# Kernel optimization log

Measured on AMD Instinct MI355X. Metric: run time of the kernel, lower is better.

The kernel has to match this reference:

```python
import jax, jax.numpy as jnp
import numpy as np

BATCH, DIN, DSTATE, SEQLEN = 4, 2048, 16, 2048


def setup_inputs() -> dict:
    key = jax.random.key(0)
    ks = jax.random.split(key, 7)
    u = jax.random.normal(ks[0], (BATCH, DIN, SEQLEN), dtype=jnp.float32)
    # delta pre-softplus; moderate positive-ish values like Mamba dt_proj output
    delta = jax.random.uniform(ks[1], (BATCH, DIN, SEQLEN), dtype=jnp.float32, minval=-2.0, maxval=1.0)
    # A is negative in real Mamba (A = -exp(A_log)); keep recurrence stable
    A = -jnp.exp(jax.random.uniform(ks[2], (DIN, DSTATE), dtype=jnp.float32, minval=-1.0, maxval=1.0))
    B = jax.random.normal(ks[3], (BATCH, DSTATE, SEQLEN), dtype=jnp.float32)
    C = jax.random.normal(ks[4], (BATCH, DSTATE, SEQLEN), dtype=jnp.float32)
    D = jax.random.normal(ks[5], (DIN,), dtype=jnp.float32)
    z = jax.random.normal(ks[6], (BATCH, DIN, SEQLEN), dtype=jnp.float32)
    return {"u": u, "delta": delta, "A": A, "B": B, "C": C, "D": D, "z": z}


def reference(u, delta, A, B, C, D, z):
    """Mamba selective scan (selective_scan_ref semantics, delta_softplus=True).

    u, delta, z: (b, d, l); A: (d, n); B, C: (b, n, l); D: (d,).
    y_t = C_t . x_t + D*u_t, x_t = exp(dt_t*A)*x_{t-1} + dt_t*B_t*u_t,
    final y gated by SiLU(z).
    """
    dt = jax.nn.softplus(delta)                      # (b, d, l)

    def step(x, inp):
        dt_t, u_t, B_t, C_t = inp                    # (b,d) (b,d) (b,n) (b,n)
        dA = jnp.exp(dt_t[..., None] * A)            # (b, d, n)
        x = x * dA + (dt_t * u_t)[..., None] * B_t[:, None, :]
        y_t = jnp.einsum('bdn,bn->bd', x, C_t)
        return x, y_t

    xs = (jnp.moveaxis(dt, -1, 0),                   # (l, b, d)
          jnp.moveaxis(u, -1, 0),
          jnp.moveaxis(B, -1, 0),                    # (l, b, n)
          jnp.moveaxis(C, -1, 0))
    x0 = jnp.zeros((u.shape[0], u.shape[1], A.shape[1]), dtype=u.dtype)
    _, ys = jax.lax.scan(step, x0, xs)               # ys: (l, b, d)
    y = jnp.moveaxis(ys, 0, -1)                      # (b, d, l)
    y = y + D[None, :, None] * u
    y = y * (z * jax.nn.sigmoid(z))                  # SiLU gate
    return y
```

## Files before the change

kernel.cpp:

```cpp
#include <hip/hip_runtime.h>


#define BATCHSZ 4
#define DIN 2048
#define NSTATE 16
#define SEQ 2048
#define NCH (BATCHSZ * DIN)
#define NGRP (NCH / 256)
#define NC 16
#define LC (SEQ / NC)
#define SUB 32
#define NSUB (LC / SUB)
#define L2E 1.44269504f

__device__ __forceinline__ float softplus_f(float v) {
    float e = __builtin_amdgcn_exp2f(v * L2E);
    return 0.69314718f * __builtin_amdgcn_logf(1.0f + e);
}

__device__ __forceinline__ float silu_f(float v) {
    float s = __builtin_amdgcn_rcpf(1.0f + __builtin_amdgcn_exp2f(-v * L2E));
    return v * s;
}

__device__ __forceinline__ float comp4(const float4& f, int k) {
    return k == 0 ? f.x : k == 1 ? f.y : k == 2 ? f.z : f.w;
}

__device__ __forceinline__ void set4(float4& f, int k, float v) {
    if (k == 0) f.x = v; else if (k == 1) f.y = v; else if (k == 2) f.z = v; else f.w = v;
}

__device__ __forceinline__ void dma16(const float* g, float* l) {
    __builtin_amdgcn_global_load_lds(
        (const __attribute__((address_space(1))) void*)g,
        (__attribute__((address_space(3))) void*)l, 16, 0, 0);
}


__global__ __launch_bounds__(256) void k_transBC(
        const float* __restrict__ Bm, const float* __restrict__ Cm,
        float* __restrict__ Bt, float* __restrict__ Ct) {
    int idx = blockIdx.x * 256 + threadIdx.x;
    int b = idx >> 11;
    int t = idx & (SEQ - 1);
    const float* sb = Bm + (size_t)b * NSTATE * SEQ + t;
    const float* sc = Cm + (size_t)b * NSTATE * SEQ + t;
    float* db = Bt + ((size_t)b * SEQ + t) * NSTATE;
    float* dc = Ct + ((size_t)b * SEQ + t) * NSTATE;
    #pragma unroll
    for (int m = 0; m < 4; ++m) {
        float4 v, w;
        v.x = sb[(size_t)(m * 4 + 0) * SEQ]; w.x = sc[(size_t)(m * 4 + 0) * SEQ];
        v.y = sb[(size_t)(m * 4 + 1) * SEQ]; w.y = sc[(size_t)(m * 4 + 1) * SEQ];
        v.z = sb[(size_t)(m * 4 + 2) * SEQ]; w.z = sc[(size_t)(m * 4 + 2) * SEQ];
        v.w = sb[(size_t)(m * 4 + 3) * SEQ]; w.w = sc[(size_t)(m * 4 + 3) * SEQ];
        *(float4*)(db + m * 4) = v;
        *(float4*)(dc + m * 4) = w;
    }
}

__global__ __launch_bounds__(256, 4) void k_pass1(
        const float* __restrict__ u, const float* __restrict__ delta,
        const float* __restrict__ A, const float* __restrict__ Bt,
        float* __restrict__ wsq, float* __restrict__ wsS) {
    __shared__ float Ub[256 * 32];
    __shared__ float Db[256 * 32];

    int tid = threadIdx.x;
    int l = tid & 63;
    int w6 = tid & ~63;
    int g = blockIdx.x & (NGRP - 1);
    int c = blockIdx.x >> 5;
    int chBase = g << 8;
    int b = chBase >> 11;
    int bd = chBase + tid;
    int d = bd & (DIN - 1);
    int rowA = w6 + (l >> 3);
    int lq = l & 7;

    const float* ug = u + (size_t)chBase * SEQ + (size_t)c * LC;
    const float* dg = delta + (size_t)chBase * SEQ + (size_t)c * LC;
    const float* Btc = Bt + ((size_t)b * SEQ + (size_t)c * LC) * NSTATE;

    float A2[NSTATE];
    {
        const float* Ar = A + (size_t)d * NSTATE;
        #pragma unroll
        for (int n = 0; n < NSTATE; ++n) A2[n] = Ar[n] * L2E;
    }
    float x[NSTATE];
    #pragma unroll
    for (int n = 0; n < NSTATE; ++n) x[n] = 0.0f;
    float S = 0.0f;

    #pragma unroll
    for (int it = 0; it < 8; ++it) {
        int r = rowA + it * 8;
        int q = lq ^ (r & 7);
        dma16(ug + (size_t)r * SEQ + q * 4, &Ub[(w6 + it * 8) * 32]);
        dma16(dg + (size_t)r * SEQ + q * 4, &Db[(w6 + it * 8) * 32]);
    }

    for (int st = 0; st < NSUB; ++st) {
        asm volatile("s_waitcnt vmcnt(0)" ::: "memory");
        __builtin_amdgcn_sched_barrier(0);
        #pragma unroll
        for (int t4 = 0; t4 < 8; ++t4) {
            int ph = (t4 ^ (tid & 7)) * 4;
            float4 u4 = *(const float4*)(&Ub[tid * 32 + ph]);
            float4 d4 = *(const float4*)(&Db[tid * 32 + ph]);
            const float4* Br = (const float4*)(Btc + (size_t)(st * SUB + t4 * 4) * NSTATE);
            #pragma unroll
            for (int k = 0; k < 4; ++k) {
                float dt = softplus_f(comp4(d4, k));
                S += dt;
                float du = dt * comp4(u4, k);
                float bb[NSTATE];
                *(float4*)&bb[0] = Br[k * 4 + 0]; *(float4*)&bb[4] = Br[k * 4 + 1];
                *(float4*)&bb[8] = Br[k * 4 + 2]; *(float4*)&bb[12] = Br[k * 4 + 3];
                #pragma unroll
                for (int n = 0; n < NSTATE; ++n) {
                    float dA = __builtin_amdgcn_exp2f(A2[n] * dt);
                    x[n] = x[n] * dA + du * bb[n];
                }
            }
        }
        if (st + 1 < NSUB) {
            __builtin_amdgcn_sched_barrier(0);
            int tb = (st + 1) * SUB;
            #pragma unroll
            for (int it = 0; it < 8; ++it) {
                int r = rowA + it * 8;
                int q = lq ^ (r & 7);
                dma16(ug + (size_t)r * SEQ + tb + q * 4, &Ub[(w6 + it * 8) * 32]);
                dma16(dg + (size_t)r * SEQ + tb + q * 4, &Db[(w6 + it * 8) * 32]);
            }
        }
    }

    #pragma unroll
    for (int n = 0; n < NSTATE; ++n) wsq[((size_t)n * NC + c) * NCH + bd] = x[n];
    wsS[(size_t)c * NCH + bd] = S;
}

__global__ __launch_bounds__(256) void k_pass2(
        const float* __restrict__ A, float* __restrict__ wsq,
        float* __restrict__ wsS) {
    int idx = blockIdx.x * 256 + threadIdx.x;
    int n = idx >> 13;
    int bd = idx & (NCH - 1);
    int d = bd & (DIN - 1);

    float A2 = A[(size_t)d * NSTATE + n] * L2E;
    float x = 0.0f;
    float* qbase = wsq + (size_t)n * NC * NCH + bd;

    #pragma unroll
    for (int c0 = 0; c0 < NC; c0 += 4) {
        float S0 = wsS[(size_t)(c0 + 0) * NCH + bd];
        float S1 = wsS[(size_t)(c0 + 1) * NCH + bd];
        float S2 = wsS[(size_t)(c0 + 2) * NCH + bd];
        float S3 = wsS[(size_t)(c0 + 3) * NCH + bd];
        float* p0 = qbase + (size_t)(c0 + 0) * NCH;
        float* p1 = qbase + (size_t)(c0 + 1) * NCH;
        float* p2 = qbase + (size_t)(c0 + 2) * NCH;
        float* p3 = qbase + (size_t)(c0 + 3) * NCH;
        float q0 = *p0, q1 = *p1, q2 = *p2, q3 = *p3;
        float t0 = x; x = x * __builtin_amdgcn_exp2f(A2 * S0) + q0;
        float t1 = x; x = x * __builtin_amdgcn_exp2f(A2 * S1) + q1;
        float t2 = x; x = x * __builtin_amdgcn_exp2f(A2 * S2) + q2;
        float t3 = x; x = x * __builtin_amdgcn_exp2f(A2 * S3) + q3;
        *p0 = t0; *p1 = t1; *p2 = t2; *p3 = t3;
    }
}

__global__ __launch_bounds__(256, 4) void k_pass3(
        const float* __restrict__ u, const float* __restrict__ delta,
        const float* __restrict__ A, const float* __restrict__ Bt,
        const float* __restrict__ Ct, const float* __restrict__ Dv,
        const float* __restrict__ z, const float* __restrict__ wsq,
        float* __restrict__ out) {
    __shared__ float Ub[256 * 32];
    __shared__ float Db[256 * 32];

    int tid = threadIdx.x;
    int l = tid & 63;
    int w6 = tid & ~63;
    int g = blockIdx.x & (NGRP - 1);
    int c = blockIdx.x >> 5;
    int chBase = g << 8;
    int b = chBase >> 11;
    int bd = chBase + tid;
    int d = bd & (DIN - 1);
    int rowA = w6 + (l >> 3);
    int lq = l & 7;

    const float* ug = u + (size_t)chBase * SEQ + (size_t)c * LC;
    const float* dg = delta + (size_t)chBase * SEQ + (size_t)c * LC;
    const float* zg = z + (size_t)chBase * SEQ + (size_t)c * LC;
    float* og = out + (size_t)chBase * SEQ + (size_t)c * LC;
    const float* Btc = Bt + ((size_t)b * SEQ + (size_t)c * LC) * NSTATE;
    const float* Ctc = Ct + ((size_t)b * SEQ + (size_t)c * LC) * NSTATE;

    float A2[NSTATE];
    {
        const float* Ar = A + (size_t)d * NSTATE;
        #pragma unroll
        for (int n = 0; n < NSTATE; ++n) A2[n] = Ar[n] * L2E;
    }
    float x[NSTATE];
    #pragma unroll
    for (int n = 0; n < NSTATE; ++n)
        x[n] = wsq[((size_t)n * NC + c) * NCH + bd];
    float Dd = Dv[d];

    #pragma unroll
    for (int it = 0; it < 8; ++it) {
        int r = rowA + it * 8;
        int q = lq ^ (r & 7);
        dma16(ug + (size_t)r * SEQ + q * 4, &Ub[(w6 + it * 8) * 32]);
        dma16(dg + (size_t)r * SEQ + q * 4, &Db[(w6 + it * 8) * 32]);
    }

    for (int st = 0; st < NSUB; ++st) {
        int tb = st * SUB;
        asm volatile("s_waitcnt vmcnt(0)" ::: "memory");
        __builtin_amdgcn_sched_barrier(0);
        #pragma unroll
        for (int t4 = 0; t4 < 8; ++t4) {
            int ph = (t4 ^ (tid & 7)) * 4;
            float4 u4 = *(const float4*)(&Ub[tid * 32 + ph]);
            float4 d4 = *(const float4*)(&Db[tid * 32 + ph]);
            const float4* Br = (const float4*)(Btc + (size_t)(tb + t4 * 4) * NSTATE);
            const float4* Cr = (const float4*)(Ctc + (size_t)(tb + t4 * 4) * NSTATE);
            float4 y4;
            #pragma unroll
            for (int k = 0; k < 4; ++k) {
                float uv = comp4(u4, k);
                float dt = softplus_f(comp4(d4, k));
                float du = dt * uv;
                float bb[NSTATE], cc[NSTATE];
                *(float4*)&bb[0] = Br[k * 4 + 0]; *(float4*)&bb[4] = Br[k * 4 + 1];
                *(float4*)&bb[8] = Br[k * 4 + 2]; *(float4*)&bb[12] = Br[k * 4 + 3];
                *(float4*)&cc[0] = Cr[k * 4 + 0]; *(float4*)&cc[4] = Cr[k * 4 + 1];
                *(float4*)&cc[8] = Cr[k * 4 + 2]; *(float4*)&cc[12] = Cr[k * 4 + 3];
                float acc = 0.0f;
                #pragma unroll
                for (int n = 0; n < NSTATE; ++n) {
                    float dA = __builtin_amdgcn_exp2f(A2[n] * dt);
                    x[n] = x[n] * dA + du * bb[n];
                    acc += x[n] * cc[n];
                }
                set4(y4, k, acc + Dd * uv);
            }
            *(float4*)(&Ub[tid * 32 + ph]) = y4;
        }
        #pragma unroll
        for (int it = 0; it < 8; ++it) {
            int r = rowA + it * 8;
            int sq = (lq ^ (r & 7)) * 4;
            float4 y4 = *(const float4*)(&Ub[r * 32 + sq]);
            float4 z4 = *(const float4*)(zg + (size_t)r * SEQ + tb + lq * 4);
            float4 oo;
            #pragma unroll
            for (int k = 0; k < 4; ++k)
                set4(oo, k, comp4(y4, k) * silu_f(comp4(z4, k)));
            *(float4*)(og + (size_t)r * SEQ + tb + lq * 4) = oo;
        }
        if (st + 1 < NSUB) {
            __builtin_amdgcn_sched_barrier(0);
            int tb2 = tb + SUB;
            #pragma unroll
            for (int it = 0; it < 8; ++it) {
                int r = rowA + it * 8;
                int q = lq ^ (r & 7);
                dma16(ug + (size_t)r * SEQ + tb2 + q * 4, &Ub[(w6 + it * 8) * 32]);
                dma16(dg + (size_t)r * SEQ + tb2 + q * 4, &Db[(w6 + it * 8) * 32]);
            }
        }
    }
}

__global__ __launch_bounds__(256) void k_simple(
        const float* __restrict__ u, const float* __restrict__ delta,
        const float* __restrict__ A, const float* __restrict__ Bm,
        const float* __restrict__ Cm, const float* __restrict__ Dv,
        const float* __restrict__ z, float* __restrict__ out) {
    int bd = blockIdx.x * 256 + threadIdx.x;
    int b  = bd >> 11;
    int d  = bd & (DIN - 1);

    float A2[NSTATE];
    const float* Ar = A + d * NSTATE;
    #pragma unroll
    for (int n = 0; n < NSTATE; ++n) A2[n] = Ar[n] * L2E;
    float x[NSTATE];
    #pragma unroll
    for (int n = 0; n < NSTATE; ++n) x[n] = 0.0f;

    float Dd = Dv[d];
    size_t base = (size_t)bd * SEQ;
    const float4* u4 = (const float4*)(u + base);
    const float4* d4 = (const float4*)(delta + base);
    const float4* z4 = (const float4*)(z + base);
    float4* o4 = (float4*)(out + base);
    const float* Bp = Bm + (size_t)b * NSTATE * SEQ;
    const float* Cp = Cm + (size_t)b * NSTATE * SEQ;

    for (int t4 = 0; t4 < SEQ / 4; ++t4) {
        float4 uu = u4[t4];
        float4 dd = d4[t4];
        float4 zz = z4[t4];
        float4 yy;
        #pragma unroll
        for (int k = 0; k < 4; ++k) {
            float uvk = comp4(uu, k);
            float dt = softplus_f(comp4(dd, k));
            float du = dt * uvk;
            int t = t4 * 4 + k;
            float acc = 0.0f;
            #pragma unroll
            for (int n = 0; n < NSTATE; ++n) {
                float dA = __builtin_amdgcn_exp2f(A2[n] * dt);
                x[n] = x[n] * dA + du * Bp[n * SEQ + t];
                acc += x[n] * Cp[n * SEQ + t];
            }
            float y = acc + Dd * uvk;
            y = y * silu_f(comp4(zz, k));
            set4(yy, k, y);
        }
        o4[t4] = yy;
    }
}

extern "C" void kernel_launch(void* const* d_in, const int* in_sizes, int n_in,
                              void* d_out, int out_size, void* d_ws, size_t ws_size,
                              hipStream_t stream) {
    const float* u     = (const float*)d_in[0];
    const float* delta = (const float*)d_in[1];
    const float* A     = (const float*)d_in[2];
    const float* Bm    = (const float*)d_in[3];
    const float* Cm    = (const float*)d_in[4];
    const float* Dv    = (const float*)d_in[5];
    const float* z     = (const float*)d_in[6];
    float* out = (float*)d_out;
    float* ws = (float*)d_ws;

    size_t nq = (size_t)NSTATE * NC * NCH;
    size_t ns = (size_t)NC * NCH;
    size_t nt = (size_t)BATCHSZ * SEQ * NSTATE;
    size_t need = (nq + ns + 2 * nt) * sizeof(float);

    if (ws_size >= need) {
        float* wsq = ws;
        float* wsS = wsq + nq;
        float* Bt  = wsS + ns;
        float* Ct  = Bt + nt;
        k_transBC<<<(BATCHSZ * SEQ) / 256, 256, 0, stream>>>(Bm, Cm, Bt, Ct);
        k_pass1<<<NGRP * NC, 256, 0, stream>>>(u, delta, A, Bt, wsq, wsS);
        k_pass2<<<(NSTATE * NCH) / 256, 256, 0, stream>>>(A, wsq, wsS);
        k_pass3<<<NGRP * NC, 256, 0, stream>>>(u, delta, A, Bt, Ct, Dv, z, wsq, out);
    } else {
        k_simple<<<NCH / 256, 256, 0, stream>>>(u, delta, A, Bm, Cm, Dv, z, out);
    }
}
```

Measured before the change: 386.9 us.

## Replace direct-to-LDS DMA with register-staged prefetch of u, delta and z

The pass1 and pass3 kernels now load the next u/delta sub-tile into registers before computing the current one, instead of issuing global_load_lds DMA after compute and waiting on vmcnt(0). The registers are written to swizzled LDS at the start of each step. Pass3 also prefetches z into registers so the gating epilogue does not stall on a global load. The aim is to overlap global-load latency with the scan compute. The extra registers push occupancy hints down from 4 to 2 blocks per CU, which may reduce latency hiding elsewhere.

```diff
diff --git a/kernel.cpp b/kernel.cpp
--- a/kernel.cpp
+++ b/kernel.cpp
@@ -31,12 +31,6 @@
     if (k == 0) f.x = v; else if (k == 1) f.y = v; else if (k == 2) f.z = v; else f.w = v;
 }
 
-__device__ __forceinline__ void dma16(const float* g, float* l) {
-    __builtin_amdgcn_global_load_lds(
-        (const __attribute__((address_space(1))) void*)g,
-        (__attribute__((address_space(3))) void*)l, 16, 0, 0);
-}
-
 
 __global__ __launch_bounds__(256) void k_transBC(
         const float* __restrict__ Bm, const float* __restrict__ Cm,
@@ -60,7 +54,7 @@
     }
 }
 
-__global__ __launch_bounds__(256, 4) void k_pass1(
+__global__ __launch_bounds__(256, 2) void k_pass1(
         const float* __restrict__ u, const float* __restrict__ delta,
         const float* __restrict__ A, const float* __restrict__ Bt,
         float* __restrict__ wsq, float* __restrict__ wsS) {
@@ -94,23 +88,37 @@
     for (int n = 0; n < NSTATE; ++n) x[n] = 0.0f;
     float S = 0.0f;
 
+    float4 ur[8], dr[8];
     #pragma unroll
     for (int it = 0; it < 8; ++it) {
         int r = rowA + it * 8;
-        int q = lq ^ (r & 7);
-        dma16(ug + (size_t)r * SEQ + q * 4, &Ub[(w6 + it * 8) * 32]);
-        dma16(dg + (size_t)r * SEQ + q * 4, &Db[(w6 + it * 8) * 32]);
+        ur[it] = *(const float4*)(ug + (size_t)r * SEQ + lq * 4);
+        dr[it] = *(const float4*)(dg + (size_t)r * SEQ + lq * 4);
     }
 
     for (int st = 0; st < NSUB; ++st) {
-        asm volatile("s_waitcnt vmcnt(0)" ::: "memory");
-        __builtin_amdgcn_sched_barrier(0);
+        int tb = st * SUB;
+        #pragma unroll
+        for (int it = 0; it < 8; ++it) {
+            int r = rowA + it * 8;
+            int p = lq ^ (r & 7);
+            *(float4*)(&Ub[r * 32 + p * 4]) = ur[it];
+            *(float4*)(&Db[r * 32 + p * 4]) = dr[it];
+        }
+        if (st + 1 < NSUB) {
+            #pragma unroll
+            for (int it = 0; it < 8; ++it) {
+                int r = rowA + it * 8;
+                ur[it] = *(const float4*)(ug + (size_t)r * SEQ + tb + SUB + lq * 4);
+                dr[it] = *(const float4*)(dg + (size_t)r * SEQ + tb + SUB + lq * 4);
+            }
+        }
         #pragma unroll
         for (int t4 = 0; t4 < 8; ++t4) {
             int ph = (t4 ^ (tid & 7)) * 4;
             float4 u4 = *(const float4*)(&Ub[tid * 32 + ph]);
             float4 d4 = *(const float4*)(&Db[tid * 32 + ph]);
-            const float4* Br = (const float4*)(Btc + (size_t)(st * SUB + t4 * 4) * NSTATE);
+            const float4* Br = (const float4*)(Btc + (size_t)(tb + t4 * 4) * NSTATE);
             #pragma unroll
             for (int k = 0; k < 4; ++k) {
                 float dt = softplus_f(comp4(d4, k));
@@ -124,17 +132,6 @@
                     float dA = __builtin_amdgcn_exp2f(A2[n] * dt);
                     x[n] = x[n] * dA + du * bb[n];
                 }
-            }
-        }
-        if (st + 1 < NSUB) {
-            __builtin_amdgcn_sched_barrier(0);
-            int tb = (st + 1) * SUB;
-            #pragma unroll
-            for (int it = 0; it < 8; ++it) {
-                int r = rowA + it * 8;
-                int q = lq ^ (r & 7);
-                dma16(ug + (size_t)r * SEQ + tb + q * 4, &Ub[(w6 + it * 8) * 32]);
-                dma16(dg + (size_t)r * SEQ + tb + q * 4, &Db[(w6 + it * 8) * 32]);
             }
         }
     }
@@ -175,7 +172,7 @@
     }
 }
 
-__global__ __launch_bounds__(256, 4) void k_pass3(
+__global__ __launch_bounds__(256, 2) void k_pass3(
         const float* __restrict__ u, const float* __restrict__ delta,
         const float* __restrict__ A, const float* __restrict__ Bt,
         const float* __restrict__ Ct, const float* __restrict__ Dv,
@@ -215,18 +212,32 @@
         x[n] = wsq[((size_t)n * NC + c) * NCH + bd];
     float Dd = Dv[d];
 
+    float4 ur[8], dr[8], zr[8];
     #pragma unroll
     for (int it = 0; it < 8; ++it) {
         int r = rowA + it * 8;
-        int q = lq ^ (r & 7);
-        dma16(ug + (size_t)r * SEQ + q * 4, &Ub[(w6 + it * 8) * 32]);
-        dma16(dg + (size_t)r * SEQ + q * 4, &Db[(w6 + it * 8) * 32]);
+        ur[it] = *(const float4*)(ug + (size_t)r * SEQ + lq * 4);
+        dr[it] = *(const float4*)(dg + (size_t)r * SEQ + lq * 4);
+        zr[it] = *(const float4*)(zg + (size_t)r * SEQ + lq * 4);
     }
 
     for (int st = 0; st < NSUB; ++st) {
         int tb = st * SUB;
-        asm volatile("s_waitcnt vmcnt(0)" ::: "memory");
-        __builtin_amdgcn_sched_barrier(0);
+        #pragma unroll
+        for (int it = 0; it < 8; ++it) {
+            int r = rowA + it * 8;
+            int p = lq ^ (r & 7);
+            *(float4*)(&Ub[r * 32 + p * 4]) = ur[it];
+            *(float4*)(&Db[r * 32 + p * 4]) = dr[it];
+        }
+        if (st + 1 < NSUB) {
+            #pragma unroll
+            for (int it = 0; it < 8; ++it) {
+                int r = rowA + it * 8;
+                ur[it] = *(const float4*)(ug + (size_t)r * SEQ + tb + SUB + lq * 4);
+                dr[it] = *(const float4*)(dg + (size_t)r * SEQ + tb + SUB + lq * 4);
+            }
+        }
         #pragma unroll
         for (int t4 = 0; t4 < 8; ++t4) {
             int ph = (t4 ^ (tid & 7)) * 4;
@@ -259,24 +270,19 @@
         #pragma unroll
         for (int it = 0; it < 8; ++it) {
             int r = rowA + it * 8;
-            int sq = (lq ^ (r & 7)) * 4;
-            float4 y4 = *(const float4*)(&Ub[r * 32 + sq]);
-            float4 z4 = *(const float4*)(zg + (size_t)r * SEQ + tb + lq * 4);
+            int p = lq ^ (r & 7);
+            float4 y4 = *(const float4*)(&Ub[r * 32 + p * 4]);
             float4 oo;
             #pragma unroll
             for (int k = 0; k < 4; ++k)
-                set4(oo, k, comp4(y4, k) * silu_f(comp4(z4, k)));
+                set4(oo, k, comp4(y4, k) * silu_f(comp4(zr[it], k)));
             *(float4*)(og + (size_t)r * SEQ + tb + lq * 4) = oo;
         }
         if (st + 1 < NSUB) {
-            __builtin_amdgcn_sched_barrier(0);
-            int tb2 = tb + SUB;
             #pragma unroll
             for (int it = 0; it < 8; ++it) {
                 int r = rowA + it * 8;
-                int q = lq ^ (r & 7);
-                dma16(ug + (size_t)r * SEQ + tb2 + q * 4, &Ub[(w6 + it * 8) * 32]);
-                dma16(dg + (size_t)r * SEQ + tb2 + q * 4, &Db[(w6 + it * 8) * 32]);
+                zr[it] = *(const float4*)(zg + (size_t)r * SEQ + tb + SUB + lq * 4);
             }
         }
     }
```

After: 378.4 us. 2.2% less time.
